# Kernel optimization log

Hardware: AMD Instinct MI355X
Metric: run time of the kernel (lower is better)

The kernel has to match this reference:

```python
import jax, jax.numpy as jnp
import numpy as np

N_NODES = 100000
N_EDGES = 1600000
HID = 128


def setup_inputs() -> dict:
    key = jax.random.key(0)
    ks = jax.random.split(key, 12)
    s = lambda fan_in: 1.0 / np.sqrt(fan_in)
    return {
        "x": jax.random.normal(ks[0], (N_NODES, HID), jnp.float32),
        "edge_index": jax.random.randint(ks[1], (2, N_EDGES), 0, N_NODES, jnp.int64),
        "edge_attr": jax.random.uniform(ks[2], (N_EDGES,), jnp.float32),
        "W_enc": jax.random.normal(ks[3], (HID, HID), jnp.float32) * s(HID),
        "b_enc": jax.random.normal(ks[4], (HID,), jnp.float32) * s(HID),
        "W_msg": jax.random.normal(ks[5], (HID + 1, HID), jnp.float32) * s(HID + 1),
        "b_msg": jax.random.normal(ks[6], (HID,), jnp.float32) * s(HID + 1),
        "W_upd": jax.random.normal(ks[7], (2 * HID, HID), jnp.float32) * s(2 * HID),
        "b_upd": jax.random.normal(ks[8], (HID,), jnp.float32) * s(2 * HID),
        "W_dec": jax.random.normal(ks[9], (HID, 1), jnp.float32) * s(HID),
        "b_dec": jax.random.normal(ks[10], (1,), jnp.float32) * s(HID),
    }


def reference(x, edge_index, edge_attr, W_enc, b_enc, W_msg, b_msg,
              W_upd, b_upd, W_dec, b_dec):
    n = x.shape[0]
    # encoder + relu
    h = jax.nn.relu(x @ W_enc + b_enc)                       # [N, H]
    src, dst = edge_index[0], edge_index[1]
    # message: gather x_j, concat scalar edge_attr, linear
    m = jnp.concatenate([h[src], edge_attr[:, None]], axis=-1) @ W_msg + b_msg  # [E, H]
    # scatter-min aggregate per destination node (nodes w/o in-edges -> 0, PyG convention)
    agg = jax.ops.segment_min(m, dst, num_segments=n)        # [N, H]
    agg = jnp.where(jnp.isinf(agg), jnp.zeros((), m.dtype), agg)
    # update: concat + linear
    u = jnp.concatenate([h, agg], axis=-1) @ W_upd + b_upd   # [N, H]
    # decoder + sigmoid
    return jax.nn.sigmoid(u @ W_dec + b_dec)                 # [N, 1]
```

## Files before the change

### kernel.cpp

```cpp
#include <hip/hip_runtime.h>

#define NN 100000
#define NE 1600000
#define HID 128
#define NBUCK 1563
#define CAP 1280
#define STP 130
#define SENT 3.0e38f
#define CH 4096
#define ENCB 391
#define MSGB 1024

typedef float f32x4 __attribute__((ext_vector_type(4)));
typedef __bf16 bf16x8 __attribute__((ext_vector_type(8)));
typedef unsigned short u16x8 __attribute__((ext_vector_type(8)));

static __device__ __forceinline__ unsigned short f2bf(float f) {
  union { float f; unsigned u; } v; v.f = f;
  unsigned u = v.u;
  return (unsigned short)((u + 0x7FFFu + ((u >> 16) & 1u)) >> 16);
}

static __device__ __forceinline__ f32x4 mfma_bf16(u16x8 a, u16x8 b, f32x4 c) {
  return __builtin_amdgcn_mfma_f32_16x16x32_bf16(
      __builtin_bit_cast(bf16x8, a), __builtin_bit_cast(bf16x8, b), c, 0, 0, 0);
}

static __device__ __forceinline__ int gidx(const int* __restrict__ ei, int is64, long long pos) {
  return is64 ? ei[pos * 2] : ei[pos];
}
static __device__ __forceinline__ int detect64(const int* __restrict__ ei, int tid) {
  unsigned long long bl = __ballot(ei[2 * (tid & 63) + 1] == 0);
  return (bl == ~0ull) ? 1 : 0;
}

__global__ __launch_bounds__(512) void k_prepw(const float* __restrict__ Wenc,
    const float* __restrict__ Wmsg, const float* __restrict__ Wupd,
    const float* __restrict__ Wdec, unsigned short* __restrict__ Wb,
    float* __restrict__ vprep, int* __restrict__ gcursor) {
  int b = blockIdx.x;
  int t = threadIdx.x;
  if (b == 96) {
    if (t < 128) {
      const float* row = Wupd + (size_t)(128 + t) * 128;
      float s = 0.f;
#pragma unroll 8
      for (int j = 0; j < 128; ++j) s = fmaf(row[j], Wdec[j], s);
      vprep[t] = s;
    }
    for (int i = t; i < NBUCK; i += 512) gcursor[i] = i * CAP;
    return;
  }
  int i = b * 512 + t;
  int m = i >> 14, idx = i & 16383;
  const float* src = (m == 0) ? Wenc : ((m == 1) ? Wmsg : Wupd);
  int k = idx >> 7, j = idx & 127;
  Wb[m * 17408 + j * 136 + k] = f2bf(src[idx]);
}

__global__ __launch_bounds__(512, 4) void k_work(const float* __restrict__ x,
    const float* __restrict__ benc, const float* __restrict__ bupd,
    const float* __restrict__ Wdec, const unsigned short* __restrict__ Wb,
    const int* __restrict__ ei, const float* __restrict__ ea,
    int* __restrict__ gcursor, unsigned long long* __restrict__ csr,
    unsigned* __restrict__ mNp, float* __restrict__ hdec) {
  __shared__ __align__(16) unsigned short Wt[17408];
  __shared__ unsigned short bounce[8][16 * 136];
  __shared__ unsigned cnt[NBUCK];
  __shared__ float bshE[128];
  __shared__ float bshU[128];
  __shared__ float wdsh[128];
  int tid = threadIdx.x;
  int eb = blockIdx.x;

  int sR[CH / 512], dR[CH / 512];
  float eaR[CH / 512];
  {
    long long base = (long long)eb * CH;
    int n = (int)(((long long)NE - base < CH) ? ((long long)NE - base) : CH);
    if (n < 0) n = 0;
    int is64 = detect64(ei, tid);
#pragma unroll
    for (int k = 0; k < CH / 512; ++k) {
      int i = k * 512 + tid;
      if (i < n) {
        sR[k] = gidx(ei, is64, base + i);
        dR[k] = gidx(ei, is64, (long long)NE + base + i);
        eaR[k] = ea[base + i];
      } else { sR[k] = 0; dR[k] = -1; eaR[k] = 0.f; }
    }
  }

  for (int i = tid; i < NBUCK; i += 512) cnt[i] = 0;
  if (tid < 128) { bshE[tid] = benc[tid]; bshU[tid] = bupd[tid]; wdsh[tid] = Wdec[tid]; }

  int wave = tid >> 6, lane = tid & 63;
  int l15 = lane & 15, lg = lane >> 4;
  f32x4 zero = {0.f, 0.f, 0.f, 0.f};
  u16x8 haG[2][4];

  for (int i = tid; i < 2176; i += 512)
    ((uint4*)Wt)[i] = ((const uint4*)Wb)[i];
  __syncthreads();
#pragma unroll
  for (int g = 0; g < 2; ++g) {
    int rowBase = eb * 256 + g * 128 + wave * 16;
    int nodeA = rowBase + l15; if (nodeA > NN - 1) nodeA = NN - 1;
    u16x8 af[4];
#pragma unroll
    for (int kt = 0; kt < 4; ++kt) {
      const float* px = x + (long long)nodeA * HID + kt * 32 + lg * 8;
      f32x4 a0 = *(const f32x4*)px;
      f32x4 a1 = *(const f32x4*)(px + 4);
      u16x8 t;
      t[0] = f2bf(a0[0]); t[1] = f2bf(a0[1]); t[2] = f2bf(a0[2]); t[3] = f2bf(a0[3]);
      t[4] = f2bf(a1[0]); t[5] = f2bf(a1[1]); t[6] = f2bf(a1[2]); t[7] = f2bf(a1[3]);
      af[kt] = t;
    }
    f32x4 acc[8];
#pragma unroll
    for (int nt = 0; nt < 8; ++nt) acc[nt] = zero;
#pragma unroll
    for (int kt = 0; kt < 4; ++kt)
#pragma unroll
      for (int nt = 0; nt < 8; ++nt) {
        u16x8 bfv = *(const u16x8*)&Wt[(nt * 16 + l15) * 136 + kt * 32 + lg * 8];
        acc[nt] = mfma_bf16(af[kt], bfv, acc[nt]);
      }
#pragma unroll
    for (int nt = 0; nt < 8; ++nt) {
      int j = nt * 16 + l15;
      float bj = bshE[j];
#pragma unroll
      for (int r = 0; r < 4; ++r) {
        float v = acc[nt][r] + bj;
        v = v > 0.f ? v : 0.f;
        bounce[wave][(lg * 4 + r) * 136 + j] = f2bf(v);
      }
    }
    asm volatile("s_waitcnt lgkmcnt(0)" ::: "memory");
    __builtin_amdgcn_sched_barrier(0);
#pragma unroll
    for (int kt = 0; kt < 4; ++kt)
      haG[g][kt] = *(const u16x8*)&bounce[wave][l15 * 136 + kt * 32 + lg * 8];
    asm volatile("s_waitcnt lgkmcnt(0)" ::: "memory");
    __builtin_amdgcn_sched_barrier(0);
  }

  unsigned long long ereg[CH / 512];
#pragma unroll
  for (int k = 0; k < CH / 512; ++k) {
    int d = dR[k];
    if (d >= 0) {
      unsigned eab = f2bf(eaR[k]);
      unsigned bkt = (unsigned)(d >> 6);
      unsigned lo = (unsigned)(sR[k] << 6) | ((unsigned)(d & 63) << 23);
      unsigned hi = (eab << 16) | bkt;
      ereg[k] = (unsigned long long)lo | ((unsigned long long)hi << 32);
      atomicAdd(&cnt[bkt], 1u);
    } else ereg[k] = 0xFFFFFFFFFFFFFFFFull;
  }
  __syncthreads();

  for (int i = tid; i < 2176; i += 512)
    ((uint4*)Wt)[i] = ((const uint4*)Wb)[2176 + i];
  __syncthreads();
#pragma unroll
  for (int g = 0; g < 2; ++g) {
    int rowBase = eb * 256 + g * 128 + wave * 16;
    f32x4 acc2[8];
#pragma unroll
    for (int nt = 0; nt < 8; ++nt) acc2[nt] = zero;
#pragma unroll
    for (int kt = 0; kt < 4; ++kt)
#pragma unroll
      for (int nt = 0; nt < 8; ++nt) {
        u16x8 bfv = *(const u16x8*)&Wt[(nt * 16 + l15) * 136 + kt * 32 + lg * 8];
        acc2[nt] = mfma_bf16(haG[g][kt], bfv, acc2[nt]);
      }
#pragma unroll
    for (int nt = 0; nt < 8; ++nt) {
      int j = nt * 16 + l15;
#pragma unroll
      for (int r = 0; r < 4; ++r)
        bounce[wave][(lg * 4 + r) * 136 + j] = f2bf(acc2[nt][r]);
    }
    asm volatile("s_waitcnt lgkmcnt(0)" ::: "memory");
    __builtin_amdgcn_sched_barrier(0);
#pragma unroll 4
    for (int row = 0; row < 16; ++row) {
      int node = rowBase + row;
      if (node < NN) {
        unsigned lo = bounce[wave][row * 136 + lane];
        unsigned hi = bounce[wave][row * 136 + 64 + lane];
        mNp[(size_t)node * 64 + lane] = lo | (hi << 16);
      }
    }
    asm volatile("s_waitcnt lgkmcnt(0)" ::: "memory");
    __builtin_amdgcn_sched_barrier(0);
  }
  __syncthreads();

  for (int i = tid; i < 2176; i += 512)
    ((uint4*)Wt)[i] = ((const uint4*)Wb)[4352 + i];
  __syncthreads();
#pragma unroll
  for (int g = 0; g < 2; ++g) {
    int rowBase = eb * 256 + g * 128 + wave * 16;
    f32x4 acc3[8];
#pragma unroll
    for (int nt = 0; nt < 8; ++nt) acc3[nt] = zero;
#pragma unroll
    for (int kt = 0; kt < 4; ++kt)
#pragma unroll
      for (int nt = 0; nt < 8; ++nt) {
        u16x8 bfv = *(const u16x8*)&Wt[(nt * 16 + l15) * 136 + kt * 32 + lg * 8];
        acc3[nt] = mfma_bf16(haG[g][kt], bfv, acc3[nt]);
      }
    float hs0 = 0.f, hs1 = 0.f, hs2 = 0.f, hs3 = 0.f;
#pragma unroll
    for (int nt = 0; nt < 8; ++nt) {
      int j = nt * 16 + l15;
      float bu = bshU[j], wv = wdsh[j];
      hs0 += (acc3[nt][0] + bu) * wv;
      hs1 += (acc3[nt][1] + bu) * wv;
      hs2 += (acc3[nt][2] + bu) * wv;
      hs3 += (acc3[nt][3] + bu) * wv;
    }
#pragma unroll
    for (int m = 1; m < 16; m <<= 1) {
      hs0 += __shfl_xor(hs0, m);
      hs1 += __shfl_xor(hs1, m);
      hs2 += __shfl_xor(hs2, m);
      hs3 += __shfl_xor(hs3, m);
    }
    if (l15 == 0) {
      int n0 = rowBase + lg * 4;
      if (n0 + 3 < NN) {
        float4 st4; st4.x = hs0; st4.y = hs1; st4.z = hs2; st4.w = hs3;
        *(float4*)&hdec[n0] = st4;
      } else {
        if (n0 + 0 < NN) hdec[n0 + 0] = hs0;
        if (n0 + 1 < NN) hdec[n0 + 1] = hs1;
        if (n0 + 2 < NN) hdec[n0 + 2] = hs2;
        if (n0 + 3 < NN) hdec[n0 + 3] = hs3;
      }
    }
  }
  __syncthreads();

  {
    unsigned* gbase = (unsigned*)&bounce[0][0];
    for (int b = tid; b < NBUCK; b += 512) {
      unsigned c = cnt[b];
      gbase[b] = c ? (unsigned)atomicAdd(&gcursor[b], (int)c) : 0u;
    }
    __syncthreads();
    for (int i = tid; i < NBUCK; i += 512) cnt[i] = 0;
    __syncthreads();
#pragma unroll
    for (int k = 0; k < CH / 512; ++k) {
      unsigned long long e = ereg[k];
      unsigned bkt = (unsigned)(e >> 32) & 0xFFFFu;
      if (bkt != 0xFFFFu) {
        unsigned lp = atomicAdd(&cnt[bkt], 1u);
        csr[gbase[bkt] + lp] = e;
      }
    }
  }
}

__global__ __launch_bounds__(512, 8) void k_msg(const unsigned* __restrict__ mNp,
    const float* __restrict__ Wmsg, const int* __restrict__ gcursor,
    const unsigned long long* __restrict__ csr, const float* __restrict__ bmsg,
    const float* __restrict__ vprep, const float* __restrict__ hdec,
    const float* __restrict__ bdec, float* __restrict__ out) {
  __shared__ float stf[64 * STP];
  int tid = threadIdx.x;
  int lane = tid & 63;
  int wv = tid >> 6;
  float wl0 = Wmsg[128 * 128 + lane];
  float wl1 = Wmsg[128 * 128 + 64 + lane];
  float vl0 = vprep[lane], vl1 = vprep[64 + lane];
  float bm0 = bmsg[lane], bm1 = bmsg[64 + lane];
  float bd = *bdec;

  for (int b = blockIdx.x; b < NBUCK; b += MSGB) {
    for (int i = tid; i < 64 * STP; i += 512) stf[i] = SENT;
    __syncthreads();

    int off = b * CAP, end = gcursor[b];
    int cntE = end - off;
    int per = (cntE + 7) >> 3;
    int i0 = off + wv * per;
    int i1 = i0 + per; if (i1 > end) i1 = end;
    int iu = __builtin_amdgcn_readfirstlane(i0);
    int ie = __builtin_amdgcn_readfirstlane(i1);

#define EDGE_DO(PK, VV) do { \
    int loc_ = (int)(((unsigned)(PK) >> 23) & 0x3Fu); \
    float ea_ = __uint_as_float((unsigned)((PK) >> 32) & 0xFFFF0000u); \
    float a0_ = fmaf(ea_, wl0, __uint_as_float((VV) << 16)); \
    float a1_ = fmaf(ea_, wl1, __uint_as_float((VV) & 0xFFFF0000u)); \
    atomicMin(&stf[loc_ * STP + lane], a0_); \
    atomicMin(&stf[loc_ * STP + 64 + lane], a1_); \
  } while (0)

    int i = iu;
    for (; i + 16 <= ie; i += 16) {
      unsigned long long pk[16];
#pragma unroll
      for (int j = 0; j < 16; ++j) pk[j] = csr[i + j];
      unsigned v[16];
#pragma unroll
      for (int j = 0; j < 16; ++j)
        v[j] = mNp[((unsigned)pk[j] & 0x7FFFFFu) + lane];
#pragma unroll
      for (int j = 0; j < 16; ++j) EDGE_DO(pk[j], v[j]);
    }
    for (; i + 4 <= ie; i += 4) {
      unsigned long long pk[4];
#pragma unroll
      for (int j = 0; j < 4; ++j) pk[j] = csr[i + j];
      unsigned v[4];
#pragma unroll
      for (int j = 0; j < 4; ++j)
        v[j] = mNp[((unsigned)pk[j] & 0x7FFFFFu) + lane];
#pragma unroll
      for (int j = 0; j < 4; ++j) EDGE_DO(pk[j], v[j]);
    }
    for (; i < ie; ++i) {
      unsigned long long pk = csr[i];
      unsigned v = mNp[((unsigned)pk & 0x7FFFFFu) + lane];
      EDGE_DO(pk, v);
    }
#undef EDGE_DO
    __syncthreads();

#pragma unroll
    for (int q = 0; q < 8; ++q) {
      int loc = (wv << 3) + q;
      float s0 = stf[loc * STP + lane];
      float s1 = stf[loc * STP + 64 + lane];
      float ps = ((s0 < 1.0e30f) ? (s0 + bm0) * vl0 : 0.f)
               + ((s1 < 1.0e30f) ? (s1 + bm1) * vl1 : 0.f);
#pragma unroll
      for (int m = 1; m < 64; m <<= 1) ps += __shfl_xor(ps, m);
      if (lane == 0) {
        int node = (b << 6) + loc;
        if (node < NN)
          out[node] = 1.f / (1.f + expf(-(ps + hdec[node] + bd)));
      }
    }
    __syncthreads();
  }
}

extern "C" void kernel_launch(void* const* d_in, const int* in_sizes, int n_in,
                              void* d_out, int out_size, void* d_ws, size_t ws_size,
                              hipStream_t stream) {
  const float* x    = (const float*)d_in[0];
  const int*   ei   = (const int*)d_in[1];
  const float* ea   = (const float*)d_in[2];
  const float* Wenc = (const float*)d_in[3];
  const float* benc = (const float*)d_in[4];
  const float* Wmsg = (const float*)d_in[5];
  const float* bmsg = (const float*)d_in[6];
  const float* Wupd = (const float*)d_in[7];
  const float* bupd = (const float*)d_in[8];
  const float* Wdec = (const float*)d_in[9];
  const float* bdec = (const float*)d_in[10];
  float* out = (float*)d_out;

  char* w = (char*)d_ws;
  auto alloc = [&](size_t bytes) { char* p = w; w += (bytes + 255) & ~(size_t)255; return p; };
  unsigned* mNp        = (unsigned*)alloc((size_t)NN * 64 * 4);
  unsigned long long* csr = (unsigned long long*)alloc((size_t)NBUCK * CAP * 8);
  unsigned short* Wb = (unsigned short*)alloc(3 * 17408 * 2);
  float* hdec   = (float*)alloc((size_t)NN * 4);
  float* vprep  = (float*)alloc(128 * 4);
  int* gcursor  = (int*)alloc((size_t)NBUCK * 4);

  k_prepw<<<97, 512, 0, stream>>>(Wenc, Wmsg, Wupd, Wdec, Wb, vprep, gcursor);
  k_work<<<ENCB, 512, 0, stream>>>(x, benc, bupd, Wdec, Wb, ei, ea,
                                   gcursor, csr, mNp, hdec);
  k_msg<<<MSGB, 512, 0, stream>>>(mNp, Wmsg, gcursor, csr, bmsg, vprep, hdec, bdec, out);
}
```

Before: 115.1 us.

## Sort bucket edges by destination in LDS and reduce runs in registers

The message kernel now runs one block per bucket and, before processing, counting-sorts each bucket's edges by local destination into a shared index array. Waves then walk the sorted indices, keep a running min in registers while the destination stays the same, and issue LDS atomicMin only when the destination changes. This is meant to cut the number of shared-memory atomics from two per edge to roughly two per destination run per wave. The cost is an extra two passes over the bucket's CSR entries plus indirect CSR loads through the sorted index.

```diff
diff --git a/kernel.cpp b/kernel.cpp
--- a/kernel.cpp
+++ b/kernel.cpp
@@ -9,7 +9,6 @@
 #define SENT 3.0e38f
 #define CH 4096
 #define ENCB 391
-#define MSGB 1024
 
 typedef float f32x4 __attribute__((ext_vector_type(4)));
 typedef __bf16 bf16x8 __attribute__((ext_vector_type(8)));
@@ -276,83 +275,117 @@
     const float* __restrict__ vprep, const float* __restrict__ hdec,
     const float* __restrict__ bdec, float* __restrict__ out) {
   __shared__ float stf[64 * STP];
+  __shared__ __align__(16) unsigned short sidx[CAP];
+  __shared__ unsigned lcnt[64];
+  __shared__ unsigned lcur[64];
+  __shared__ unsigned pbase[64];
   int tid = threadIdx.x;
+  int b = blockIdx.x;
   int lane = tid & 63;
   int wv = tid >> 6;
+  for (int i = tid; i < 64 * STP; i += 512) stf[i] = SENT;
+  if (tid < 64) { lcnt[tid] = 0; lcur[tid] = 0; }
+  __syncthreads();
+
+  int off = b * CAP, end = gcursor[b];
+  int cntE = end - off;
+  const unsigned* csr32 = (const unsigned*)csr;
+
+  for (int i = tid; i < cntE; i += 512) {
+    unsigned lo = csr32[(size_t)(off + i) * 2];
+    atomicAdd(&lcnt[(lo >> 23) & 63u], 1u);
+  }
+  __syncthreads();
+  if (tid < 64) {
+    unsigned v = lcnt[tid];
+    unsigned run = v;
+#pragma unroll
+    for (int m = 1; m < 64; m <<= 1) {
+      unsigned t = __shfl_up(run, m);
+      if (lane >= m) run += t;
+    }
+    pbase[tid] = run - v;
+  }
+  __syncthreads();
+  for (int i = tid; i < cntE; i += 512) {
+    unsigned lo = csr32[(size_t)(off + i) * 2];
+    unsigned loc = (lo >> 23) & 63u;
+    unsigned p = atomicAdd(&lcur[loc], 1u);
+    sidx[pbase[loc] + p] = (unsigned short)i;
+  }
+  __syncthreads();
+
+  int per = (((cntE + 7) >> 3) + 7) & ~7;
+  int k0 = wv * per; if (k0 > cntE) k0 = cntE;
+  int k1 = k0 + per; if (k1 > cntE) k1 = cntE;
+  k0 = __builtin_amdgcn_readfirstlane(k0);
+  k1 = __builtin_amdgcn_readfirstlane(k1);
   float wl0 = Wmsg[128 * 128 + lane];
   float wl1 = Wmsg[128 * 128 + 64 + lane];
+  int cur = -1;
+  float m0 = SENT, m1 = SENT;
+
+#define PROC(E, V) do { \
+    int loc_ = __builtin_amdgcn_readfirstlane((int)(((unsigned)(E) >> 23) & 63u)); \
+    float ea_ = __uint_as_float((unsigned)((E) >> 32) & 0xFFFF0000u); \
+    float a0_ = fmaf(ea_, wl0, __uint_as_float((V) << 16)); \
+    float a1_ = fmaf(ea_, wl1, __uint_as_float((V) & 0xFFFF0000u)); \
+    if (loc_ != cur) { \
+      if (cur >= 0) { \
+        atomicMin(&stf[cur * STP + lane], m0); \
+        atomicMin(&stf[cur * STP + 64 + lane], m1); \
+      } \
+      cur = loc_; m0 = a0_; m1 = a1_; \
+    } else { m0 = fminf(m0, a0_); m1 = fminf(m1, a1_); } \
+  } while (0)
+
+  int k = k0;
+  for (; k + 8 <= k1; k += 8) {
+    uint4 iw = *(const uint4*)&sidx[k];
+    unsigned w[4] = {iw.x, iw.y, iw.z, iw.w};
+    unsigned long long e[8];
+    unsigned v[8];
+#pragma unroll
+    for (int j = 0; j < 8; ++j) {
+      unsigned si = (w[j >> 1] >> ((j & 1) * 16)) & 0xFFFFu;
+      e[j] = csr[off + (int)si];
+    }
+#pragma unroll
+    for (int j = 0; j < 8; ++j)
+      v[j] = mNp[((unsigned)e[j] & 0x7FFFFFu) + lane];
+#pragma unroll
+    for (int j = 0; j < 8; ++j) PROC(e[j], v[j]);
+  }
+  for (; k < k1; ++k) {
+    unsigned si = sidx[k];
+    unsigned long long e = csr[off + (int)si];
+    unsigned v = mNp[((unsigned)e & 0x7FFFFFu) + lane];
+    PROC(e, v);
+  }
+#undef PROC
+  if (cur >= 0) {
+    atomicMin(&stf[cur * STP + lane], m0);
+    atomicMin(&stf[cur * STP + 64 + lane], m1);
+  }
+  __syncthreads();
+
   float vl0 = vprep[lane], vl1 = vprep[64 + lane];
   float bm0 = bmsg[lane], bm1 = bmsg[64 + lane];
   float bd = *bdec;
-
-  for (int b = blockIdx.x; b < NBUCK; b += MSGB) {
-    for (int i = tid; i < 64 * STP; i += 512) stf[i] = SENT;
-    __syncthreads();
-
-    int off = b * CAP, end = gcursor[b];
-    int cntE = end - off;
-    int per = (cntE + 7) >> 3;
-    int i0 = off + wv * per;
-    int i1 = i0 + per; if (i1 > end) i1 = end;
-    int iu = __builtin_amdgcn_readfirstlane(i0);
-    int ie = __builtin_amdgcn_readfirstlane(i1);
-
-#define EDGE_DO(PK, VV) do { \
-    int loc_ = (int)(((unsigned)(PK) >> 23) & 0x3Fu); \
-    float ea_ = __uint_as_float((unsigned)((PK) >> 32) & 0xFFFF0000u); \
-    float a0_ = fmaf(ea_, wl0, __uint_as_float((VV) << 16)); \
-    float a1_ = fmaf(ea_, wl1, __uint_as_float((VV) & 0xFFFF0000u)); \
-    atomicMin(&stf[loc_ * STP + lane], a0_); \
-    atomicMin(&stf[loc_ * STP + 64 + lane], a1_); \
-  } while (0)
-
-    int i = iu;
-    for (; i + 16 <= ie; i += 16) {
-      unsigned long long pk[16];
-#pragma unroll
-      for (int j = 0; j < 16; ++j) pk[j] = csr[i + j];
-      unsigned v[16];
-#pragma unroll
-      for (int j = 0; j < 16; ++j)
-        v[j] = mNp[((unsigned)pk[j] & 0x7FFFFFu) + lane];
-#pragma unroll
-      for (int j = 0; j < 16; ++j) EDGE_DO(pk[j], v[j]);
-    }
-    for (; i + 4 <= ie; i += 4) {
-      unsigned long long pk[4];
-#pragma unroll
-      for (int j = 0; j < 4; ++j) pk[j] = csr[i + j];
-      unsigned v[4];
-#pragma unroll
-      for (int j = 0; j < 4; ++j)
-        v[j] = mNp[((unsigned)pk[j] & 0x7FFFFFu) + lane];
-#pragma unroll
-      for (int j = 0; j < 4; ++j) EDGE_DO(pk[j], v[j]);
-    }
-    for (; i < ie; ++i) {
-      unsigned long long pk = csr[i];
-      unsigned v = mNp[((unsigned)pk & 0x7FFFFFu) + lane];
-      EDGE_DO(pk, v);
-    }
-#undef EDGE_DO
-    __syncthreads();
-
-#pragma unroll
-    for (int q = 0; q < 8; ++q) {
-      int loc = (wv << 3) + q;
-      float s0 = stf[loc * STP + lane];
-      float s1 = stf[loc * STP + 64 + lane];
-      float ps = ((s0 < 1.0e30f) ? (s0 + bm0) * vl0 : 0.f)
-               + ((s1 < 1.0e30f) ? (s1 + bm1) * vl1 : 0.f);
-#pragma unroll
-      for (int m = 1; m < 64; m <<= 1) ps += __shfl_xor(ps, m);
-      if (lane == 0) {
-        int node = (b << 6) + loc;
-        if (node < NN)
-          out[node] = 1.f / (1.f + expf(-(ps + hdec[node] + bd)));
-      }
-    }
-    __syncthreads();
+#pragma unroll
+  for (int q = 0; q < 8; ++q) {
+    int loc = (wv << 3) + q;
+    float s0 = stf[loc * STP + lane];
+    float s1 = stf[loc * STP + 64 + lane];
+    float ps = ((s0 < 1.0e30f) ? (s0 + bm0) * vl0 : 0.f)
+             + ((s1 < 1.0e30f) ? (s1 + bm1) * vl1 : 0.f);
+#pragma unroll
+    for (int m = 1; m < 64; m <<= 1) ps += __shfl_xor(ps, m);
+    if (lane == 0) {
+      int node = (b << 6) + loc;
+      if (node < NN)
+        out[node] = 1.f / (1.f + expf(-(ps + hdec[node] + bd)));
+    }
   }
 }
 
@@ -384,5 +417,5 @@
   k_prepw<<<97, 512, 0, stream>>>(Wenc, Wmsg, Wupd, Wdec, Wb, vprep, gcursor);
   k_work<<<ENCB, 512, 0, stream>>>(x, benc, bupd, Wdec, Wb, ei, ea,
                                    gcursor, csr, mNp, hdec);
-  k_msg<<<MSGB, 512, 0, stream>>>(mNp, Wmsg, gcursor, csr, bmsg, vprep, hdec, bdec, out);
-}
+  k_msg<<<NBUCK, 512, 0, stream>>>(mNp, Wmsg, gcursor, csr, bmsg, vprep, hdec, bdec, out);
+}
```

Measured after the change: 132.3 us. 1.15x slower.
